# Performance work log

Hardware: AMD Instinct MI355X
Metric: run time of the kernel (lower is better)

The kernel has to match this reference:

```python
import jax, jax.numpy as jnp
from jax import lax
import numpy as np

B, N, F_IN = 8, 8192, 64
NPOINT, K = 2048, 16
C0 = F_IN + 3  # use_xyz concat
EPS = 1e-5


def setup_inputs() -> dict:
    key = jax.random.key(0)
    ks = jax.random.split(key, 8)
    xyz = jax.random.normal(ks[0], (B, 3, N), dtype=jnp.float32)
    points = jax.random.normal(ks[1], (B, F_IN, N), dtype=jnp.float32)
    def conv_params(k, cout, cin):
        W = jax.random.normal(k, (cout, cin), dtype=jnp.float32) * (1.0 / np.sqrt(cin))
        return W, jnp.zeros((cout,), jnp.float32)
    W1, b1 = conv_params(ks[2], 64, C0)
    W2, b2 = conv_params(ks[3], 64, 64)
    W3, b3 = conv_params(ks[4], 128, 64)
    g1 = jnp.ones((64,), jnp.float32); be1 = jnp.zeros((64,), jnp.float32)
    g2 = jnp.ones((64,), jnp.float32); be2 = jnp.zeros((64,), jnp.float32)
    return dict(xyz=xyz, points=points, W1=W1, b1=b1, g1=g1, be1=be1,
                W2=W2, b2=b2, g2=g2, be2=be2, W3=W3, b3=b3)


def _fps(xyz_bn3, npoint):
    # furthest point sampling; starts at index 0 (as PointNet++ CUDA op)
    b, n, _ = xyz_bn3.shape
    init_idx = jnp.zeros((b,), jnp.int32)
    dist0 = jnp.full((b, n), 1e10, xyz_bn3.dtype)

    def body(carry, _):
        dist, last = carry
        p = jnp.take_along_axis(xyz_bn3, last[:, None, None], axis=1)  # (b,1,3)
        d = jnp.sum((xyz_bn3 - p) ** 2, axis=-1)                       # (b,n)
        dist = jnp.minimum(dist, d)
        nxt = jnp.argmax(dist, axis=-1).astype(jnp.int32)
        return (dist, nxt), nxt

    (_, _), rest = lax.scan(body, (dist0, init_idx), None, length=npoint - 1)
    return jnp.concatenate([init_idx[None], rest], axis=0).T  # (b, npoint)


def _gather_feat(feat, idx):
    # feat: (B,C,N), idx: (B,...) -> (B,C,...)
    return jax.vmap(lambda f, i: f[:, i])(feat, idx)


def _conv_bn_relu(x, W, b, g, be):
    # 1x1 Conv2d + BatchNorm2d(training batch stats) + ReLU
    y = jnp.einsum('oi,bipk->bopk', W, x) + b[None, :, None, None]
    mean = y.mean(axis=(0, 2, 3))
    var = y.var(axis=(0, 2, 3))
    y = (y - mean[None, :, None, None]) * lax.rsqrt(var + EPS)[None, :, None, None]
    y = y * g[None, :, None, None] + be[None, :, None, None]
    return jax.nn.relu(y)


def reference(xyz, points, W1, b1, g1, be1, W2, b2, g2, be2, W3, b3):
    # --- sample_and_group_knn ---
    xyz_t = jnp.transpose(xyz, (0, 2, 1))             # (B,N,3)
    fps_idx = _fps(xyz_t, NPOINT)                      # (B,npoint)
    new_xyz = _gather_feat(xyz, fps_idx)               # (B,3,npoint)
    q = jnp.transpose(new_xyz, (0, 2, 1))              # (B,npoint,3)
    # squared distances (B,npoint,N)
    sq = (jnp.sum(q ** 2, -1)[:, :, None]
          + jnp.sum(xyz_t ** 2, -1)[:, None, :]
          - 2.0 * jnp.einsum('bqc,bnc->bqn', q, xyz_t))
    _, idx = lax.top_k(-sq, K)                         # (B,npoint,K) nearest
    grouped_xyz = _gather_feat(xyz, idx)               # (B,3,npoint,K)
    grouped_xyz = grouped_xyz - new_xyz[:, :, :, None]
    grouped_pts = _gather_feat(points, idx)            # (B,f,npoint,K)
    new_points = jnp.concatenate([grouped_xyz, grouped_pts], axis=1)  # (B,67,npoint,K)
    # --- shared MLP (1x1 convs) + max-pool over neighbors ---
    h = _conv_bn_relu(new_points, W1, b1, g1, be1)
    h = _conv_bn_relu(h, W2, b2, g2, be2)
    h = jnp.einsum('oi,bipk->bopk', W3, h) + b3[None, :, None, None]  # no bn/act
    new_feat = jnp.max(h, axis=3)                      # (B,128,npoint)
    return new_xyz, new_feat
```

## Files before the change

kernel.cpp:

```cpp
#include <hip/hip_runtime.h>
#pragma clang fp contract(off)

#define BB 8
#define NN 8192
#define NP 2048
#define KNbr 16
#define FIN 64
#define NPOS (BB*NP*KNbr)
#define NCONS 248
#define AG __HIP_MEMORY_SCOPE_AGENT

typedef float f32x2 __attribute__((ext_vector_type(2)));
typedef unsigned long long u64;

__device__ __forceinline__ float sq3(float x, float y, float z) {
  return __fadd_rn(__fadd_rn(__fmul_rn(x,x), __fmul_rn(y,y)), __fmul_rn(z,z));
}

__device__ __forceinline__ int wave_imax(int x) {
  x = max(x, __builtin_amdgcn_update_dpp(0, x, 0x111, 0xf, 0xf, false));
  x = max(x, __builtin_amdgcn_update_dpp(0, x, 0x112, 0xf, 0xf, false));
  x = max(x, __builtin_amdgcn_update_dpp(0, x, 0x114, 0xf, 0xf, false));
  x = max(x, __builtin_amdgcn_update_dpp(0, x, 0x118, 0xf, 0xf, false));
  x = max(x, __builtin_amdgcn_update_dpp(0, x, 0x142, 0xa, 0xf, false));
  x = max(x, __builtin_amdgcn_update_dpp(0, x, 0x143, 0xc, 0xf, false));
  return __builtin_amdgcn_readlane(x, 63);
}
__device__ __forceinline__ unsigned wave_umin(unsigned x) {
  x = min(x, (unsigned)__builtin_amdgcn_update_dpp(-1, (int)x, 0x111, 0xf, 0xf, false));
  x = min(x, (unsigned)__builtin_amdgcn_update_dpp(-1, (int)x, 0x112, 0xf, 0xf, false));
  x = min(x, (unsigned)__builtin_amdgcn_update_dpp(-1, (int)x, 0x114, 0xf, 0xf, false));
  x = min(x, (unsigned)__builtin_amdgcn_update_dpp(-1, (int)x, 0x118, 0xf, 0xf, false));
  x = min(x, (unsigned)__builtin_amdgcn_update_dpp(-1, (int)x, 0x142, 0xa, 0xf, false));
  x = min(x, (unsigned)__builtin_amdgcn_update_dpp(-1, (int)x, 0x143, 0xc, 0xf, false));
  return (unsigned)__builtin_amdgcn_readlane((int)x, 63);
}

__global__ __launch_bounds__(256,1) void k_front2(const float* __restrict__ xyz,
                                                  const float* __restrict__ pts,
                                                  const float* __restrict__ W1,
                                                  const float* __restrict__ b1,
                                                  float4* __restrict__ xyzw,
                                                  float* __restrict__ qwf,
                                                  float* __restrict__ pre,
                                                  float* __restrict__ stats,
                                                  float* __restrict__ st2p,
                                                  int* __restrict__ prog,
                                                  int* __restrict__ pflag,
                                                  float* __restrict__ ybuf,
                                                  float* __restrict__ newxyz) {
  __shared__ float tx[NN], ty[NN], tz[NN];
  __shared__ float4 res[NP];
  __shared__ u64 skey[2][4];
  int blk = blockIdx.x, tid = threadIdx.x;
  int lane = tid & 63, wave = tid >> 6;

  if (blk >= 8) {
    for (int g = (blk-8)*256 + tid; g < BB*NN; g += NCONS*256) {
      int b = g >> 13, n = g & (NN-1);
      const float* p = xyz + (size_t)b*3*NN;
      float x = p[n], y = p[NN+n], z = p[2*NN+n];
      xyzw[g] = make_float4(x, y, z, sq3(x,y,z));
      const float* P = pts + (size_t)b*FIN*NN + n;
      float pv[64];
      #pragma unroll
      for (int i=0;i<64;++i) pv[i] = P[(size_t)i*NN];
      float4* outp = (float4*)(pre + (size_t)g*64);
      for (int og=0; og<16; ++og) {
        float acc[4];
        #pragma unroll
        for (int oo=0;oo<4;++oo) {
          int o = og*4+oo;
          float s = b1[o];
          #pragma unroll
          for (int i=0;i<64;++i) s = fmaf(W1[o*67+3+i], pv[i], s);
          acc[oo] = s;
        }
        outp[og] = make_float4(acc[0],acc[1],acc[2],acc[3]);
      }
    }
    if (blk == 8) stats[tid] = 0.f;
    if (blk >= 8 && blk < 24) st2p[(blk-8)*256 + tid] = 0.f;
    __syncthreads();
    if (tid == 0) {
      __threadfence();
      __hip_atomic_store(&pflag[blk-8], 1, __ATOMIC_RELEASE, AG);
    }
    bool ok = false;
    while (!ok) {
      int v = 1;
      for (int i = lane; i < NCONS; i += 64)
        v &= (__hip_atomic_load(&pflag[i], __ATOMIC_RELAXED, AG) == 1);
      ok = (bool)__all(v);
      if (!ok) __builtin_amdgcn_s_sleep(32);
    }
    __threadfence();

    int slot = (blk-8)*4 + wave;
    float W1a = W1[lane*67+0], W1b = W1[lane*67+1], W1c = W1[lane*67+2];
    float sum = 0.f, ss = 0.f;
    for (int qi = slot; qi < BB*NP; qi += NCONS*4) {
      int t = qi >> 3, b = qi & 7;
      while (__hip_atomic_load(&prog[b*32], __ATOMIC_RELAXED, AG) <= t)
        __builtin_amdgcn_s_sleep(16);
      const float* qp = qwf + ((size_t)(b*NP + t))*4;
      float qx  = __hip_atomic_load(qp+0, __ATOMIC_RELAXED, AG);
      float qy  = __hip_atomic_load(qp+1, __ATOMIC_RELAXED, AG);
      float qz  = __hip_atomic_load(qp+2, __ATOMIC_RELAXED, AG);
      float qw4 = __hip_atomic_load(qp+3, __ATOMIC_RELAXED, AG);
      const float4* base = xyzw + (size_t)b*NN;
      float ld = 3.0e38f; int li = 0x7fffffff;
      float taud = 3.0e38f; int taui = 0x7fffffff;
      for (int c = 0; c < 128; ++c) {
        int idx = c*64 + lane;
        float4 P = base[idx];
        float dot = __fadd_rn(__fadd_rn(__fmul_rn(P.x,qx), __fmul_rn(P.y,qy)), __fmul_rn(P.z,qz));
        float dd  = __fsub_rn(__fadd_rn(qw4, P.w), __fmul_rn(2.0f, dot));
        bool better = (dd < taud) || (dd == taud && idx < taui);
        u64 mask = __ballot(better);
        while (mask) {
          int src = __ffsll(mask) - 1;
          mask &= mask - 1;
          float bd = __shfl(dd, src, 64);
          int   bi = __shfl(idx, src, 64);
          bool before = (ld < bd) || (ld == bd && li < bi);
          float sd = __shfl_up(ld, 1, 64);
          int   si = __shfl_up(li, 1, 64);
          int   bp = __shfl_up((int)before, 1, 64);
          bool take_new = !before && (lane == 0 || bp);
          float nd = before ? ld : (take_new ? bd : sd);
          int   ni = before ? li : (take_new ? bi : si);
          if (lane < 16) { ld = nd; li = ni; }
          taud = __shfl(ld, 15, 64);
          taui = __shfl(li, 15, 64);
        }
      }
      const float* preb = pre + (size_t)b*NN*64;
      float* yb = ybuf + ((size_t)(b*NP + t))*16*64;
      for (int l=0;l<16;++l) {
        int n = __shfl(li, l, 64);
        float4 P = base[n];
        float dx=__fsub_rn(P.x,qx), dy=__fsub_rn(P.y,qy), dz=__fsub_rn(P.z,qz);
        float v = fmaf(W1a, dx, fmaf(W1b, dy, fmaf(W1c, dz, preb[(size_t)n*64 + lane])));
        yb[l*64 + lane] = v;
        sum += v; ss = fmaf(v, v, ss);
      }
    }
    atomicAdd(&stats[lane], sum);
    atomicAdd(&stats[64+lane], ss);
    return;
  }

  int b = blk;
  const float* pxyz = xyz + (size_t)b*3*NN;
  f32x2 px[16], py[16], pz[16], d2[16];
  #pragma unroll
  for (int j=0;j<16;++j) {
    int i = j*512 + 2*tid;
    float2 xv = *(const float2*)(pxyz + i);
    float2 yv = *(const float2*)(pxyz + NN + i);
    float2 zv = *(const float2*)(pxyz + 2*NN + i);
    tx[i] = xv.x; tx[i+1] = xv.y;
    ty[i] = yv.x; ty[i+1] = yv.y;
    tz[i] = zv.x; tz[i+1] = zv.y;
    px[j] = f32x2{xv.x, xv.y};
    py[j] = f32x2{yv.x, yv.y};
    pz[j] = f32x2{zv.x, zv.y};
    d2[j] = f32x2{1e10f, 1e10f};
  }
  float cx = pxyz[0], cy = pxyz[NN], cz = pxyz[2*NN];
  if (tid==0) {
    res[0] = make_float4(cx, cy, cz, 0.f);
    __hip_atomic_store(qwf + (size_t)(b*NP)*4 + 0, cx, __ATOMIC_RELAXED, AG);
    __hip_atomic_store(qwf + (size_t)(b*NP)*4 + 1, cy, __ATOMIC_RELAXED, AG);
    __hip_atomic_store(qwf + (size_t)(b*NP)*4 + 2, cz, __ATOMIC_RELAXED, AG);
    __hip_atomic_store(qwf + (size_t)(b*NP)*4 + 3, sq3(cx,cy,cz), __ATOMIC_RELAXED, AG);
    __hip_atomic_store(&prog[b*32], 1, __ATOMIC_RELEASE, AG);
  }
  int w = tid>>6;
  __syncthreads();
  for (int t=1;t<NP;++t) {
    f32x2 cx2 = {cx,cx}, cy2 = {cy,cy}, cz2 = {cz,cz};
    #pragma unroll
    for (int j=0;j<16;++j) {
      f32x2 dx = px[j]-cx2, dy = py[j]-cy2, dz = pz[j]-cz2;
      f32x2 dd = (dx*dx + dy*dy) + dz*dz;
#if __has_builtin(__builtin_elementwise_min)
      d2[j] = __builtin_elementwise_min(d2[j], dd);
#else
      d2[j].x = fminf(d2[j].x, dd.x);
      d2[j].y = fminf(d2[j].y, dd.y);
#endif
    }
    float tv[16]; int tk[16];
    #pragma unroll
    for (int j=0;j<16;++j) {
      bool r = d2[j].y > d2[j].x;
      tv[j] = r ? d2[j].y : d2[j].x;
      tk[j] = r ? 2*j+1 : 2*j;
    }
    #pragma unroll
    for (int j=0;j<8;++j) { bool r = tv[j+8] > tv[j]; if (r){tv[j]=tv[j+8]; tk[j]=tk[j+8];} }
    #pragma unroll
    for (int j=0;j<4;++j) { bool r = tv[j+4] > tv[j]; if (r){tv[j]=tv[j+4]; tk[j]=tk[j+4];} }
    #pragma unroll
    for (int j=0;j<2;++j) { bool r = tv[j+2] > tv[j]; if (r){tv[j]=tv[j+2]; tk[j]=tk[j+2];} }
    bool rr = tv[1] > tv[0];
    float lmax = rr ? tv[1] : tv[0];
    int   k    = rr ? tk[1] : tk[0];
    unsigned gidx = (unsigned)((k>>1)*512 + 2*tid + (k&1));
    int mb = wave_imax(__float_as_int(lmax));
    unsigned cand = (__float_as_int(lmax) == mb) ? gidx : 0xFFFFFFFFu;
    unsigned wwin = wave_umin(cand);
    int buf = t & 1;
    if ((tid & 63) == 0)
      skey[buf][w] = ((u64)(unsigned)mb << 32) | (u64)(0xFFFFFFFFu - wwin);
    __syncthreads();
    if ((t & 63) == 0) {
      int e = t - 64 + (tid >> 2), comp = tid & 3;
      float4 r = res[e];
      float v = (comp==0) ? r.x : (comp==1) ? r.y : (comp==2) ? r.z : sq3(r.x,r.y,r.z);
      __hip_atomic_store(qwf + ((size_t)(b*NP + e))*4 + comp, v, __ATOMIC_RELAXED, AG);
    } else if ((t & 63) == 1 && t > 64 && tid == 0) {
      __hip_atomic_store(&prog[b*32], t-1, __ATOMIC_RELEASE, AG);
    }
    u64 mk = skey[buf][0];
    if (skey[buf][1] > mk) mk = skey[buf][1];
    if (skey[buf][2] > mk) mk = skey[buf][2];
    if (skey[buf][3] > mk) mk = skey[buf][3];
    unsigned widx = 0xFFFFFFFFu - (unsigned)(mk & 0xFFFFFFFFull);
    cx = tx[widx]; cy = ty[widx]; cz = tz[widx];
    if (tid == (t & 255))
      res[t] = make_float4(cx, cy, cz, 0.f);
  }
  __syncthreads();
  float* outx = newxyz + (size_t)b*3*NP;
  #pragma unroll
  for (int s=0;s<8;++s) {
    int i = s*256 + tid;
    float4 r = res[i];
    *(float4*)(qwf + ((size_t)(b*NP + i))*4) = make_float4(r.x, r.y, r.z, sq3(r.x,r.y,r.z));
    outx[i] = r.x; outx[NP + i] = r.y; outx[2*NP + i] = r.z;
  }
  __syncthreads();
  if (tid == 0) {
    __threadfence();
    __hip_atomic_store(&prog[b*32], NP, __ATOMIC_RELEASE, AG);
  }
}

__device__ __forceinline__ float dot64(const float4* x, const float* W, float init) {
  float a0 = init, a1 = 0.f, a2 = 0.f, a3 = 0.f;
  #pragma unroll
  for (int j=0;j<16;++j) {
    float4 v = x[j];
    a0 = fmaf(v.x, W[4*j],   a0);
    a1 = fmaf(v.y, W[4*j+1], a1);
    a2 = fmaf(v.z, W[4*j+2], a2);
    a3 = fmaf(v.w, W[4*j+3], a3);
  }
  return (a0+a1)+(a2+a3);
}

__global__ __launch_bounds__(256) void k_conv2f(float* __restrict__ y,
                                                const float* __restrict__ W2,
                                                const float* __restrict__ b2,
                                                const float* __restrict__ st1,
                                                const float* __restrict__ g1,
                                                const float* __restrict__ be1,
                                                float* __restrict__ st2p) {
  __shared__ __align__(16) float4 xs[1024];
  __shared__ __align__(16) float sS[64], sT[64];
  __shared__ float r1[4][64], r2[4][64];
  int tid = threadIdx.x, lane = tid & 63, wave = tid >> 6;
  if (tid < 64) {
    float mean = st1[tid] * (1.0f/NPOS);
    float var  = st1[64+tid] * (1.0f/NPOS) - mean*mean;
    float istd = 1.0f / sqrtf(var + 1e-5f);
    float s = g1[tid]*istd;
    sS[tid] = s;
    sT[tid] = be1[tid] - mean*s;
  }
  float W[64];
  #pragma unroll
  for (int j=0;j<16;++j) {
    float4 t = *(const float4*)(W2 + (size_t)lane*64 + j*4);
    W[4*j]=t.x; W[4*j+1]=t.y; W[4*j+2]=t.z; W[4*j+3]=t.w;
  }
  float bb = b2[lane];
  __syncthreads();
  size_t tbase = (size_t)blockIdx.x * 1024;
  float4* Y4 = (float4*)y;
  #pragma unroll
  for (int i=0;i<4;++i) {
    int idx = i*256 + tid;
    float4 v = Y4[tbase + idx];
    int c0 = (idx & 15)*4;
    float4 s4 = *(const float4*)(sS + c0);
    float4 t4 = *(const float4*)(sT + c0);
    v.x = fmaxf(0.f, fmaf(v.x, s4.x, t4.x));
    v.y = fmaxf(0.f, fmaf(v.y, s4.y, t4.y));
    v.z = fmaxf(0.f, fmaf(v.z, s4.z, t4.z));
    v.w = fmaxf(0.f, fmaf(v.w, s4.w, t4.w));
    xs[idx] = v;
  }
  __syncthreads();
  float sum = 0.f, ss = 0.f;
  size_t pos0 = (size_t)blockIdx.x*64 + wave*16;
  #pragma unroll 1
  for (int p=0;p<16;++p) {
    float acc = dot64(&xs[(wave*16+p)*16], W, bb);
    y[(pos0+p)*64 + lane] = acc;
    sum += acc; ss = fmaf(acc, acc, ss);
  }
  r1[wave][lane] = sum; r2[wave][lane] = ss;
  __syncthreads();
  if (tid < 64) {
    float t1 = r1[0][tid]+r1[1][tid]+r1[2][tid]+r1[3][tid];
    float t2 = r2[0][tid]+r2[1][tid]+r2[2][tid]+r2[3][tid];
    float* bank = st2p + (blockIdx.x & 31)*128;
    atomicAdd(&bank[tid], t1);
    atomicAdd(&bank[64+tid], t2);
  }
}

__global__ __launch_bounds__(256) void k_c3f(const float* __restrict__ y,
                                             const float* __restrict__ W3,
                                             const float* __restrict__ b3,
                                             const float* __restrict__ st2p,
                                             const float* __restrict__ g2,
                                             const float* __restrict__ be2,
                                             float* __restrict__ feat) {
  __shared__ __align__(16) float4 xs[1024];
  __shared__ __align__(16) float sS[64], sT[64];
  int tid = threadIdx.x, lane = tid & 63, wave = tid >> 6;
  int h = wave & 1, qpair = wave >> 1;
  if (tid < 64) {
    float s1 = 0.f, s2 = 0.f;
    #pragma unroll
    for (int k=0;k<32;++k) {
      s1 += st2p[k*128 + tid];
      s2 += st2p[k*128 + 64 + tid];
    }
    float mean = s1 * (1.0f/NPOS);
    float var  = s2 * (1.0f/NPOS) - mean*mean;
    float istd = 1.0f / sqrtf(var + 1e-5f);
    float s = g2[tid]*istd;
    sS[tid] = s;
    sT[tid] = be2[tid] - mean*s;
  }
  int O = h*64 + lane;
  float W[64];
  #pragma unroll
  for (int j=0;j<16;++j) {
    float4 t = *(const float4*)(W3 + (size_t)O*64 + j*4);
    W[4*j]=t.x; W[4*j+1]=t.y; W[4*j+2]=t.z; W[4*j+3]=t.w;
  }
  float bb = b3[O];
  __syncthreads();
  size_t tbase = (size_t)blockIdx.x * 1024;
  const float4* Y4 = (const float4*)y;
  #pragma unroll
  for (int i=0;i<4;++i) {
    int idx = i*256 + tid;
    float4 v = Y4[tbase + idx];
    int c0 = (idx & 15)*4;
    float4 s4 = *(const float4*)(sS + c0);
    float4 t4 = *(const float4*)(sT + c0);
    v.x = fmaxf(0.f, fmaf(v.x, s4.x, t4.x));
    v.y = fmaxf(0.f, fmaf(v.y, s4.y, t4.y));
    v.z = fmaxf(0.f, fmaf(v.z, s4.z, t4.z));
    v.w = fmaxf(0.f, fmaf(v.w, s4.w, t4.w));
    xs[idx] = v;
  }
  __syncthreads();
  float mq[2];
  #pragma unroll 1
  for (int q=0;q<2;++q) {
    float m = -3.0e38f;
    #pragma unroll 1
    for (int k=0;k<16;++k) {
      int p = (qpair*2 + q)*16 + k;
      m = fmaxf(m, dot64(&xs[p*16], W, bb));
    }
    mq[q] = m;
  }
  int gq0 = blockIdx.x*4 + qpair*2;
  int b = gq0 >> 11, qq = gq0 & (NP-1);
  float* fp = feat + ((size_t)(b*128 + O))*NP + qq;
  fp[0] = mq[0];
  fp[1] = mq[1];
}

extern "C" void kernel_launch(void* const* d_in, const int* in_sizes, int n_in,
                              void* d_out, int out_size, void* d_ws, size_t ws_size,
                              hipStream_t stream) {
  const float* xyz = (const float*)d_in[0];
  const float* pts = (const float*)d_in[1];
  const float* W1  = (const float*)d_in[2];
  const float* b1  = (const float*)d_in[3];
  const float* g1  = (const float*)d_in[4];
  const float* be1 = (const float*)d_in[5];
  const float* W2  = (const float*)d_in[6];
  const float* b2  = (const float*)d_in[7];
  const float* g2  = (const float*)d_in[8];
  const float* be2 = (const float*)d_in[9];
  const float* W3  = (const float*)d_in[10];
  const float* b3  = (const float*)d_in[11];
  float* out = (float*)d_out;
  float* ws  = (float*)d_ws;

  float4* xyzw  = (float4*)ws;
  float*  qwf   = ws + 262144;
  float*  pre   = ws + 1654784;
  float*  ybuf  = ws + 5849088;
  float*  stats = ws + 22626304;
  float*  st2p  = ws + 22626560;
  int*    prog  = (int*)(ws + 22630656);
  int*    pflag = (int*)(ws + 22630912);

  k_front2<<<256, 256, 0, stream>>>(xyz, pts, W1, b1, xyzw, qwf, pre, stats, st2p,
                                    prog, pflag, ybuf, out);
  k_conv2f<<<4096, 256, 0, stream>>>(ybuf, W2, b2, stats, g1, be1, st2p);
  k_c3f   <<<4096, 256, 0, stream>>>(ybuf, W3, b3, st2p, g2, be2, out + 49152);
}
```

Before: 2.276 ms.

## Transpose conv2/conv3 mapping: lane per position, weights via uniform loads

The conv2 and conv3 kernels change from one lane per output channel, with per-lane weight registers, to one lane per spatial position. Each lane holds its 64-element input row in registers, and each wave loops over a subset of output channels, reading weight rows through wave-uniform (scalar-friendly) loads. LDS layouts are XOR-swizzled to avoid bank conflicts. Conv2 stages its output in a transposed LDS buffer for coalesced stores and channel statistics. Conv3 does the neighbor max with DPP row reductions and writes float4 results. This is meant to cut VGPR pressure and LDS reads, at the cost of extra LDS space and swizzle arithmetic.

```diff
diff --git a/kernel.cpp b/kernel.cpp
--- a/kernel.cpp
+++ b/kernel.cpp
@@ -249,20 +249,7 @@
   }
 }
 
-__device__ __forceinline__ float dot64(const float4* x, const float* W, float init) {
-  float a0 = init, a1 = 0.f, a2 = 0.f, a3 = 0.f;
-  #pragma unroll
-  for (int j=0;j<16;++j) {
-    float4 v = x[j];
-    a0 = fmaf(v.x, W[4*j],   a0);
-    a1 = fmaf(v.y, W[4*j+1], a1);
-    a2 = fmaf(v.z, W[4*j+2], a2);
-    a3 = fmaf(v.w, W[4*j+3], a3);
-  }
-  return (a0+a1)+(a2+a3);
-}
-
-__global__ __launch_bounds__(256) void k_conv2f(float* __restrict__ y,
+__global__ __launch_bounds__(256) void k_conv2t(float* __restrict__ y,
                                                 const float* __restrict__ W2,
                                                 const float* __restrict__ b2,
                                                 const float* __restrict__ st1,
@@ -270,6 +257,7 @@
                                                 const float* __restrict__ be1,
                                                 float* __restrict__ st2p) {
   __shared__ __align__(16) float4 xs[1024];
+  __shared__ float ys[4096];
   __shared__ __align__(16) float sS[64], sT[64];
   __shared__ float r1[4][64], r2[4][64];
   int tid = threadIdx.x, lane = tid & 63, wave = tid >> 6;
@@ -281,13 +269,6 @@
     sS[tid] = s;
     sT[tid] = be1[tid] - mean*s;
   }
-  float W[64];
-  #pragma unroll
-  for (int j=0;j<16;++j) {
-    float4 t = *(const float4*)(W2 + (size_t)lane*64 + j*4);
-    W[4*j]=t.x; W[4*j+1]=t.y; W[4*j+2]=t.z; W[4*j+3]=t.w;
-  }
-  float bb = b2[lane];
   __syncthreads();
   size_t tbase = (size_t)blockIdx.x * 1024;
   float4* Y4 = (float4*)y;
@@ -302,18 +283,49 @@
     v.y = fmaxf(0.f, fmaf(v.y, s4.y, t4.y));
     v.z = fmaxf(0.f, fmaf(v.z, s4.z, t4.z));
     v.w = fmaxf(0.f, fmaf(v.w, s4.w, t4.w));
-    xs[idx] = v;
-  }
-  __syncthreads();
-  float sum = 0.f, ss = 0.f;
-  size_t pos0 = (size_t)blockIdx.x*64 + wave*16;
+    int pos = idx >> 4, j = idx & 15;
+    xs[pos*16 + (j ^ (pos & 15))] = v;
+  }
+  __syncthreads();
+  float4 x4[16];
+  #pragma unroll
+  for (int j=0;j<16;++j) x4[j] = xs[lane*16 + (j ^ (lane & 15))];
+  int cb = wave*16;
   #pragma unroll 1
+  for (int cc=0; cc<16; ++cc) {
+    int c = cb + cc;
+    const float4* Wr = (const float4*)(W2 + (size_t)c*64);
+    float a0 = b2[c], a1 = 0.f, a2 = 0.f, a3 = 0.f;
+    #pragma unroll
+    for (int j=0;j<16;++j) {
+      float4 wv = Wr[j];
+      a0 = fmaf(x4[j].x, wv.x, a0);
+      a1 = fmaf(x4[j].y, wv.y, a1);
+      a2 = fmaf(x4[j].z, wv.z, a2);
+      a3 = fmaf(x4[j].w, wv.w, a3);
+    }
+    ys[c*64 + ((lane ^ c) & 63)] = (a0+a1)+(a2+a3);
+  }
+  __syncthreads();
+  #pragma unroll
+  for (int i=0;i<4;++i) {
+    int idx = i*256 + tid;
+    int pos = idx >> 4, c0 = (idx & 15)*4;
+    float4 v;
+    v.x = ys[(c0+0)*64 + ((pos ^ (c0+0)) & 63)];
+    v.y = ys[(c0+1)*64 + ((pos ^ (c0+1)) & 63)];
+    v.z = ys[(c0+2)*64 + ((pos ^ (c0+2)) & 63)];
+    v.w = ys[(c0+3)*64 + ((pos ^ (c0+3)) & 63)];
+    Y4[tbase + idx] = v;
+  }
+  float s1 = 0.f, s2 = 0.f;
+  #pragma unroll
   for (int p=0;p<16;++p) {
-    float acc = dot64(&xs[(wave*16+p)*16], W, bb);
-    y[(pos0+p)*64 + lane] = acc;
-    sum += acc; ss = fmaf(acc, acc, ss);
-  }
-  r1[wave][lane] = sum; r2[wave][lane] = ss;
+    int pos = wave*16 + p;
+    float v = ys[lane*64 + ((pos ^ lane) & 63)];
+    s1 += v; s2 = fmaf(v, v, s2);
+  }
+  r1[wave][lane] = s1; r2[wave][lane] = s2;
   __syncthreads();
   if (tid < 64) {
     float t1 = r1[0][tid]+r1[1][tid]+r1[2][tid]+r1[3][tid];
@@ -324,7 +336,7 @@
   }
 }
 
-__global__ __launch_bounds__(256) void k_c3f(const float* __restrict__ y,
+__global__ __launch_bounds__(256) void k_c3t(const float* __restrict__ y,
                                              const float* __restrict__ W3,
                                              const float* __restrict__ b3,
                                              const float* __restrict__ st2p,
@@ -332,9 +344,9 @@
                                              const float* __restrict__ be2,
                                              float* __restrict__ feat) {
   __shared__ __align__(16) float4 xs[1024];
+  __shared__ __align__(16) float4 fs[128];
   __shared__ __align__(16) float sS[64], sT[64];
   int tid = threadIdx.x, lane = tid & 63, wave = tid >> 6;
-  int h = wave & 1, qpair = wave >> 1;
   if (tid < 64) {
     float s1 = 0.f, s2 = 0.f;
     #pragma unroll
@@ -349,14 +361,6 @@
     sS[tid] = s;
     sT[tid] = be2[tid] - mean*s;
   }
-  int O = h*64 + lane;
-  float W[64];
-  #pragma unroll
-  for (int j=0;j<16;++j) {
-    float4 t = *(const float4*)(W3 + (size_t)O*64 + j*4);
-    W[4*j]=t.x; W[4*j+1]=t.y; W[4*j+2]=t.z; W[4*j+3]=t.w;
-  }
-  float bb = b3[O];
   __syncthreads();
   size_t tbase = (size_t)blockIdx.x * 1024;
   const float4* Y4 = (const float4*)y;
@@ -371,25 +375,41 @@
     v.y = fmaxf(0.f, fmaf(v.y, s4.y, t4.y));
     v.z = fmaxf(0.f, fmaf(v.z, s4.z, t4.z));
     v.w = fmaxf(0.f, fmaf(v.w, s4.w, t4.w));
-    xs[idx] = v;
-  }
-  __syncthreads();
-  float mq[2];
+    int pos = idx >> 4, j = idx & 15;
+    xs[pos*16 + (j ^ (pos & 15))] = v;
+  }
+  __syncthreads();
+  float4 x4[16];
+  #pragma unroll
+  for (int j=0;j<16;++j) x4[j] = xs[lane*16 + (j ^ (lane & 15))];
+  int cb = wave*32;
   #pragma unroll 1
-  for (int q=0;q<2;++q) {
-    float m = -3.0e38f;
-    #pragma unroll 1
-    for (int k=0;k<16;++k) {
-      int p = (qpair*2 + q)*16 + k;
-      m = fmaxf(m, dot64(&xs[p*16], W, bb));
-    }
-    mq[q] = m;
-  }
-  int gq0 = blockIdx.x*4 + qpair*2;
-  int b = gq0 >> 11, qq = gq0 & (NP-1);
-  float* fp = feat + ((size_t)(b*128 + O))*NP + qq;
-  fp[0] = mq[0];
-  fp[1] = mq[1];
+  for (int cc=0; cc<32; ++cc) {
+    int c = cb + cc;
+    const float4* Wr = (const float4*)(W3 + (size_t)c*64);
+    float a0 = b3[c], a1 = 0.f, a2 = 0.f, a3 = 0.f;
+    #pragma unroll
+    for (int j=0;j<16;++j) {
+      float4 wv = Wr[j];
+      a0 = fmaf(x4[j].x, wv.x, a0);
+      a1 = fmaf(x4[j].y, wv.y, a1);
+      a2 = fmaf(x4[j].z, wv.z, a2);
+      a3 = fmaf(x4[j].w, wv.w, a3);
+    }
+    float m = (a0+a1)+(a2+a3);
+    m = fmaxf(m, __int_as_float(__builtin_amdgcn_update_dpp(__float_as_int(m), __float_as_int(m), 0x111, 0xf, 0xf, false)));
+    m = fmaxf(m, __int_as_float(__builtin_amdgcn_update_dpp(__float_as_int(m), __float_as_int(m), 0x112, 0xf, 0xf, false)));
+    m = fmaxf(m, __int_as_float(__builtin_amdgcn_update_dpp(__float_as_int(m), __float_as_int(m), 0x114, 0xf, 0xf, false)));
+    m = fmaxf(m, __int_as_float(__builtin_amdgcn_update_dpp(__float_as_int(m), __float_as_int(m), 0x118, 0xf, 0xf, false)));
+    if ((lane & 15) == 15) ((float*)fs)[c*4 + (lane >> 4)] = m;
+  }
+  __syncthreads();
+  if (tid < 128) {
+    float4 v = fs[tid];
+    int gq0 = blockIdx.x*4;
+    int b = gq0 >> 11, qq = gq0 & (NP-1);
+    *(float4*)(feat + ((size_t)(b*128 + tid))*NP + qq) = v;
+  }
 }
 
 extern "C" void kernel_launch(void* const* d_in, const int* in_sizes, int n_in,
@@ -421,6 +441,6 @@
 
   k_front2<<<256, 256, 0, stream>>>(xyz, pts, W1, b1, xyzw, qwf, pre, stats, st2p,
                                     prog, pflag, ybuf, out);
-  k_conv2f<<<4096, 256, 0, stream>>>(ybuf, W2, b2, stats, g1, be1, st2p);
-  k_c3f   <<<4096, 256, 0, stream>>>(ybuf, W3, b3, st2p, g2, be2, out + 49152);
-}
+  k_conv2t<<<4096, 256, 0, stream>>>(ybuf, W2, b2, stats, g1, be1, st2p);
+  k_c3t   <<<4096, 256, 0, stream>>>(ybuf, W3, b3, st2p, g2, be2, out + 49152);
+}
```

New measurement: 2.473 ms. 8.6% more time.
